# Performance work log

Measured on AMD Instinct MI355X. Metric: run time of the kernel, lower is better.

Reference implementation:

```python
import jax, jax.numpy as jnp
import numpy as np

N_NODES = 100000
N_EDGES = 1600000
IN_FEATS = 64
HIDDEN = 64
NUM_CLASSES = 40


def setup_inputs() -> dict:
    key = jax.random.key(0)
    ks = jax.random.split(key, 8)
    x = jax.random.normal(ks[0], (N_NODES, IN_FEATS), dtype=jnp.float32)
    edge_index = jax.random.randint(ks[1], (2, N_EDGES), 0, N_NODES, dtype=jnp.int64)
    s = 1.0 / np.sqrt(IN_FEATS)
    W1_l = jax.random.uniform(ks[2], (HIDDEN, IN_FEATS), jnp.float32, -s, s)
    b1 = jnp.zeros((HIDDEN,), jnp.float32)
    W1_r = jax.random.uniform(ks[3], (HIDDEN, IN_FEATS), jnp.float32, -s, s)
    s2 = 1.0 / np.sqrt(HIDDEN)
    W2_l = jax.random.uniform(ks[4], (NUM_CLASSES, HIDDEN), jnp.float32, -s2, s2)
    b2 = jnp.zeros((NUM_CLASSES,), jnp.float32)
    W2_r = jax.random.uniform(ks[5], (NUM_CLASSES, HIDDEN), jnp.float32, -s2, s2)
    return {"x": x, "edge_index": edge_index, "W1_l": W1_l, "b1": b1,
            "W1_r": W1_r, "W2_l": W2_l, "b2": b2, "W2_r": W2_r}


def _sage_conv(x, src, dst, Wl, b, Wr, num_nodes):
    # mean aggregation of source-node features onto target nodes
    msg = x[src]                                           # [E, d] gather
    agg = jax.ops.segment_sum(msg, dst, num_segments=num_nodes)   # [N, d]
    deg = jax.ops.segment_sum(jnp.ones((src.shape[0],), x.dtype), dst,
                              num_segments=num_nodes)      # [N]
    agg = agg / jnp.maximum(deg, 1.0)[:, None]
    # out = lin_l(agg) + lin_r(x)  (PyG SAGEConv: root weight, bias on lin_l)
    return agg @ Wl.T + b + x @ Wr.T


def reference(x, edge_index, W1_l, b1, W1_r, W2_l, b2, W2_r):
    n = x.shape[0]
    src, dst = edge_index[0], edge_index[1]
    h = _sage_conv(x, src, dst, W1_l, b1, W1_r, n)
    h = jax.nn.relu(h)
    # dropout p=0.5 only active in training; reference runs eval mode (identity)
    return _sage_conv(h, src, dst, W2_l, b2, W2_r, n)
```

## Files before the change

kernel.cpp:

```cpp
#include <hip/hip_runtime.h>

#define N_NODES 100000
#define N_EDGES 1600000
#define NCLS 40
#define BIN_SH 8
#define BIN_N 256
#define NBIN ((N_NODES + BIN_N - 1) / BIN_N)
#define BINCAP 4800
#define BKBLK 256
#define BKTHR 1024
#define CHUNK (N_EDGES / BKBLK)
#define SENTINEL N_NODES
#define NN1 (N_NODES + 1)

typedef __attribute__((ext_vector_type(8))) short s8v;
typedef __attribute__((ext_vector_type(4))) float f4v;

__device__ __forceinline__ unsigned short f2bf(float f) {
    union { float f; unsigned int u; } v; v.f = f;
    unsigned int u = v.u + 0x7FFFu + ((v.u >> 16) & 1u);
    return (unsigned short)(u >> 16);
}
__device__ __forceinline__ float blo(unsigned int u) {
    union { unsigned int u; float f; } v; v.u = u << 16; return v.f;
}
__device__ __forceinline__ float bhi(unsigned int u) {
    union { unsigned int u; float f; } v; v.u = u & 0xFFFF0000u; return v.f;
}

#if __has_builtin(__builtin_amdgcn_cvt_pk_fp8_f32) && __has_builtin(__builtin_amdgcn_cvt_f32_fp8)
#define FP8_HW 1
#else
#define FP8_HW 0
#endif

__device__ __forceinline__ unsigned char enc_e4m3_sw(float f) {
    union { float f; unsigned int u; } v; v.f = f;
    unsigned int s = (v.u >> 24) & 0x80u;
    float af = fabsf(f);
    if (af >= 448.0f) return (unsigned char)(s | 0x7E);
    if (af < 0.015625f) {
        int q = (int)rintf(af * 512.0f);
        return (unsigned char)(s | (q & 7));
    }
    unsigned int n = v.u & 0x7FFFFFFFu;
    n = n + 0x7FFFFu + ((n >> 20) & 1u);
    int e = (int)(n >> 23) - 120;
    unsigned int m = (n >> 20) & 7u;
    if (e <= 0) { int q = (int)rintf(af * 512.0f); return (unsigned char)(s | (q & 7)); }
    if (e > 15) return (unsigned char)(s | 0x7E);
    return (unsigned char)(s | (e << 3) | m);
}
__device__ __forceinline__ float dec_e4m3_sw(unsigned int byte) {
    unsigned int sgn = byte >> 7, e = (byte >> 3) & 15u, m = byte & 7u;
    float mag;
    if (e) { union { unsigned int u; float f; } v; v.u = ((e + 120u) << 23) | (m << 20); mag = v.f; }
    else mag = (float)m * 0.001953125f;
    return sgn ? -mag : mag;
}

__device__ __forceinline__ unsigned int pack4_fp8(float a, float b, float c, float d) {
#if FP8_HW
    unsigned int w = __builtin_amdgcn_cvt_pk_fp8_f32(a, b, 0u, false);
    w = __builtin_amdgcn_cvt_pk_fp8_f32(c, d, w, true);
    return w;
#else
    return (unsigned int)enc_e4m3_sw(a) | ((unsigned int)enc_e4m3_sw(b) << 8) |
           ((unsigned int)enc_e4m3_sw(c) << 16) | ((unsigned int)enc_e4m3_sw(d) << 24);
#endif
}
__device__ __forceinline__ void unpack4_fp8(unsigned int w, float& a, float& b, float& c, float& d) {
#if FP8_HW
    a = __builtin_amdgcn_cvt_f32_fp8(w, 0);
    b = __builtin_amdgcn_cvt_f32_fp8(w, 1);
    c = __builtin_amdgcn_cvt_f32_fp8(w, 2);
    d = __builtin_amdgcn_cvt_f32_fp8(w, 3);
#else
    a = dec_e4m3_sw(w & 255u); b = dec_e4m3_sw((w >> 8) & 255u);
    c = dec_e4m3_sw((w >> 16) & 255u); d = dec_e4m3_sw(w >> 24);
#endif
}

__global__ __launch_bounds__(BKTHR) void k_bucket(
        const int* __restrict__ srcv, const int* __restrict__ dstv,
        int* __restrict__ bcur, int* __restrict__ bedges) {
    __shared__ int cnt4[4][NBIN];
    __shared__ int base[NBIN], lcur[NBIN];
    for (int i = threadIdx.x; i < 4 * NBIN; i += BKTHR) cnt4[i / NBIN][i % NBIN] = 0;
    __syncthreads();
    const int grp = threadIdx.x >> 8;
    const int beg = blockIdx.x * CHUNK;
    const int end = beg + CHUNK;
    for (int e = beg + threadIdx.x; e < end; e += BKTHR) {
        int d = dstv[e]; d = min(max(d, 0), N_NODES - 1);
        atomicAdd(&cnt4[grp][d >> BIN_SH], 1);
    }
    __syncthreads();
    for (int i = threadIdx.x; i < NBIN; i += BKTHR) {
        int c = cnt4[0][i] + cnt4[1][i] + cnt4[2][i] + cnt4[3][i];
        base[i] = atomicAdd(&bcur[i], c);
        lcur[i] = 0;
    }
    __syncthreads();
    for (int e = beg + threadIdx.x; e < end; e += BKTHR) {
        int d = dstv[e]; d = min(max(d, 0), N_NODES - 1);
        int s = srcv[e]; s = min(max(s, 0), N_NODES - 1);
        int b = d >> BIN_SH;
        int slot = atomicAdd(&lcur[b], 1) + base[b];
        if (slot < BINCAP) bedges[b * BINCAP + slot] = ((d & (BIN_N - 1)) << 17) | s;
    }
}

__global__ __launch_bounds__(256) void k_csrfill(
        const int* __restrict__ bcur, const int* __restrict__ bedges,
        int* __restrict__ gcnt, uint2* __restrict__ offdeg,
        int* __restrict__ srcs) {
    __shared__ int dcnt[BIN_N];
    __shared__ int s[BIN_N];
    __shared__ int base_s;
    const int b = blockIdx.x;
    dcnt[threadIdx.x] = 0;
    __syncthreads();
    const int cnt = min(bcur[b], BINCAP);
    for (int e = threadIdx.x; e < cnt; e += 256)
        atomicAdd(&dcnt[bedges[b * BINCAP + e] >> 17], 1);
    __syncthreads();
    int v = dcnt[threadIdx.x];
    int pv = (v + 3) & ~3;
    s[threadIdx.x] = pv;
    __syncthreads();
    int acc = pv;
    for (int off = 1; off < 256; off <<= 1) {
        int t = (threadIdx.x >= off) ? s[threadIdx.x - off] : 0;
        __syncthreads();
        acc += t;
        s[threadIdx.x] = acc;
        __syncthreads();
    }
    if (threadIdx.x == 255) base_s = atomicAdd(gcnt, acc);
    __syncthreads();
    const int gbeg = (acc - pv) + base_s;
    const int node = (b << BIN_SH) + threadIdx.x;
    if (node < N_NODES) offdeg[node] = make_uint2((unsigned)gbeg, (unsigned)v);
    s[threadIdx.x] = gbeg;
    dcnt[threadIdx.x] = 0;
    __syncthreads();
    for (int e = threadIdx.x; e < cnt; e += 256) {
        int val = bedges[b * BINCAP + e];
        int dl = val >> 17;
        int sv = val & 0x1FFFF;
        int slot = atomicAdd(&dcnt[dl], 1);
        srcs[s[dl] + slot] = sv;
    }
    for (int p = v; p < pv; ++p) srcs[gbeg + p] = SENTINEL;
}

__global__ void k_xb(const float* __restrict__ x, unsigned int* __restrict__ xbs,
                     unsigned int* __restrict__ h2f8) {
    int i = blockIdx.x * blockDim.x + threadIdx.x;
    int stride = gridDim.x * blockDim.x;
    const int total = N_NODES * 8;
    for (int tt = i; tt < total; tt += stride) {
        int node = tt >> 3, sub = tt & 7;
        int slice = sub >> 1, half = sub & 1;
        float4 v0 = ((const float4*)x)[tt * 2];
        float4 v1 = ((const float4*)x)[tt * 2 + 1];
        uint4 o;
        o.x = (unsigned)f2bf(v0.x) | ((unsigned)f2bf(v0.y) << 16);
        o.y = (unsigned)f2bf(v0.z) | ((unsigned)f2bf(v0.w) << 16);
        o.z = (unsigned)f2bf(v1.x) | ((unsigned)f2bf(v1.y) << 16);
        o.w = (unsigned)f2bf(v1.z) | ((unsigned)f2bf(v1.w) << 16);
        ((uint4*)xbs)[((size_t)slice * NN1 + node) * 2 + half] = o;
    }
    uint4 z; z.x = 0u; z.y = 0u; z.z = 0u; z.w = 0u;
    if (i < 8) {
        int slice = i >> 1, half = i & 1;
        ((uint4*)xbs)[((size_t)slice * NN1 + N_NODES) * 2 + half] = z;
    }
    if (i >= 16 && i < 24) h2f8[(size_t)N_NODES * 8 + (i - 16)] = 0u;
    if (i >= 24 && i < 26) h2f8[8 * (size_t)NN1 + (size_t)N_NODES * 2 + (i - 24)] = 0u;
}

__global__ __launch_bounds__(256) void k_agg(
        const uint2* __restrict__ offdeg, const int* __restrict__ srcs,
        const unsigned short* __restrict__ xbs, unsigned short* __restrict__ aggs) {
    const int lane = threadIdx.x & 63;
    const int w = threadIdx.x >> 6;
    const int g = lane >> 4;
    const int c = (lane >> 2) & 3;
    const int t = lane & 3;
    const int slice = (blockIdx.x & 7) >> 1;
    const int cid = ((blockIdx.x >> 3) << 1) | (blockIdx.x & 1);
    const size_t sb = (size_t)slice * NN1;
    for (int nb = (cid * 4 + w) * 4; nb < N_NODES; nb += 8192) {
        const int node = nb + g;
        uint2 od = offdeg[node];
        const int beg = (int)od.x;
        const int m = ((int)od.y + 3) >> 2;
        float ax = 0.0f, ay = 0.0f, az = 0.0f, aw = 0.0f;
        int j = c;
        if (j < m) {
            int4 sv = *(const int4*)&srcs[beg + 4 * j];
            while (true) {
                const int4 cur = sv;
                const int jn = j + 4;
                if (jn < m) sv = *(const int4*)&srcs[beg + 4 * jn];
                uint2 u0 = *(const uint2*)&xbs[(sb + cur.x) * 16 + t * 4];
                uint2 u1 = *(const uint2*)&xbs[(sb + cur.y) * 16 + t * 4];
                uint2 u2 = *(const uint2*)&xbs[(sb + cur.z) * 16 + t * 4];
                uint2 u3 = *(const uint2*)&xbs[(sb + cur.w) * 16 + t * 4];
                ax += (blo(u0.x) + blo(u1.x)) + (blo(u2.x) + blo(u3.x));
                ay += (bhi(u0.x) + bhi(u1.x)) + (bhi(u2.x) + bhi(u3.x));
                az += (blo(u0.y) + blo(u1.y)) + (blo(u2.y) + blo(u3.y));
                aw += (bhi(u0.y) + bhi(u1.y)) + (bhi(u2.y) + bhi(u3.y));
                if (jn >= m) break;
                j = jn;
            }
        }
        ax += __shfl_xor(ax, 4, 64); ay += __shfl_xor(ay, 4, 64);
        az += __shfl_xor(az, 4, 64); aw += __shfl_xor(aw, 4, 64);
        ax += __shfl_xor(ax, 8, 64); ay += __shfl_xor(ay, 8, 64);
        az += __shfl_xor(az, 8, 64); aw += __shfl_xor(aw, 8, 64);
        if (c == 0) {
            float rd = 1.0f / fmaxf((float)od.y, 1.0f);
            uint2 r;
            r.x = (unsigned)f2bf(ax * rd) | ((unsigned)f2bf(ay * rd) << 16);
            r.y = (unsigned)f2bf(az * rd) | ((unsigned)f2bf(aw * rd) << 16);
            *(uint2*)&aggs[(sb + node) * 16 + t * 4] = r;
        }
    }
}

__global__ __launch_bounds__(256) void k_dense(
        const unsigned short* __restrict__ aggs, const unsigned short* __restrict__ xbs,
        const float* __restrict__ W1l, const float* __restrict__ b1,
        const float* __restrict__ W1r,
        const float* __restrict__ W2l, const float* __restrict__ b2,
        const float* __restrict__ W2r,
        unsigned int* __restrict__ h2f8, float* __restrict__ op) {
    __shared__ __align__(16) unsigned short wl1[64][72], wr1[64][72];
    __shared__ __align__(16) unsigned short wl2[48][72], wr2[48][72];
    __shared__ __align__(16) unsigned short hsm[4][16][72];
    for (int idx = threadIdx.x; idx < 64 * 64; idx += 256) {
        int f = idx >> 6, k = idx & 63;
        wl1[f][k] = f2bf(W1l[idx]);
        wr1[f][k] = f2bf(W1r[idx]);
    }
    for (int idx = threadIdx.x; idx < 48 * 64; idx += 256) {
        int c = idx >> 6, k = idx & 63;
        wl2[c][k] = (c < NCLS) ? f2bf(W2l[c * 64 + k]) : (unsigned short)0;
        wr2[c][k] = (c < NCLS) ? f2bf(W2r[c * 64 + k]) : (unsigned short)0;
    }
    __syncthreads();
    const int w   = threadIdx.x >> 6;
    const int l15 = threadIdx.x & 15;
    const int g   = (threadIdx.x >> 4) & 3;
    const size_t sLo = (size_t)(g >> 1) * NN1;
    const size_t sHi = (size_t)(2 + (g >> 1)) * NN1;
    const int off = (g & 1) * 8;
    float b1v[4][4], b2v[3][4];
    #pragma unroll
    for (int ft = 0; ft < 4; ++ft)
        #pragma unroll
        for (int r = 0; r < 4; ++r)
            b1v[ft][r] = b1[16 * ft + 4 * g + r];
    #pragma unroll
    for (int ct = 0; ct < 3; ++ct)
        #pragma unroll
        for (int r = 0; r < 4; ++r) {
            int c = 16 * ct + 4 * g + r;
            b2v[ct][r] = (c < NCLS) ? b2[c] : 0.0f;
        }
    unsigned short* hs = &hsm[w][0][0];
    const int gw = blockIdx.x * 4 + w;
    const int nw = gridDim.x * 4;
    for (int tile = gw; tile < N_NODES / 16; tile += nw) {
        const size_t node = (size_t)tile * 16 + l15;
        s8v aB0 = *(const s8v*)&aggs[(sLo + node) * 16 + off];
        s8v aB1 = *(const s8v*)&aggs[(sHi + node) * 16 + off];
        s8v xB0 = *(const s8v*)&xbs[(sLo + node) * 16 + off];
        s8v xB1 = *(const s8v*)&xbs[(sHi + node) * 16 + off];
        #pragma unroll
        for (int ft = 0; ft < 4; ++ft) {
            f4v c;
            c[0] = b1v[ft][0]; c[1] = b1v[ft][1]; c[2] = b1v[ft][2]; c[3] = b1v[ft][3];
            const size_t rb = (size_t)(16 * ft + l15) * 144 + 16 * g;
            s8v A0 = *(const s8v*)((const char*)wl1 + rb);
            s8v A1 = *(const s8v*)((const char*)wl1 + rb + 64);
            s8v R0 = *(const s8v*)((const char*)wr1 + rb);
            s8v R1 = *(const s8v*)((const char*)wr1 + rb + 64);
            c = __builtin_amdgcn_mfma_f32_16x16x32_bf16(A0, aB0, c, 0, 0, 0);
            c = __builtin_amdgcn_mfma_f32_16x16x32_bf16(A1, aB1, c, 0, 0, 0);
            c = __builtin_amdgcn_mfma_f32_16x16x32_bf16(R0, xB0, c, 0, 0, 0);
            c = __builtin_amdgcn_mfma_f32_16x16x32_bf16(R1, xB1, c, 0, 0, 0);
            uint2 u;
            u.x = (unsigned)f2bf(fmaxf(c[0], 0.0f)) | ((unsigned)f2bf(fmaxf(c[1], 0.0f)) << 16);
            u.y = (unsigned)f2bf(fmaxf(c[2], 0.0f)) | ((unsigned)f2bf(fmaxf(c[3], 0.0f)) << 16);
            *(uint2*)((char*)hs + l15 * 144 + 32 * ft + 8 * g) = u;
        }
        s8v hB0 = *(const s8v*)((const char*)hs + l15 * 144 + 16 * g);
        s8v hB1 = *(const s8v*)((const char*)hs + l15 * 144 + 64 + 16 * g);
        #pragma unroll
        for (int ct = 0; ct < 3; ++ct) {
            f4v p; p[0] = 0.0f; p[1] = 0.0f; p[2] = 0.0f; p[3] = 0.0f;
            f4v qv;
            qv[0] = b2v[ct][0]; qv[1] = b2v[ct][1]; qv[2] = b2v[ct][2]; qv[3] = b2v[ct][3];
            const size_t rb = (size_t)(16 * ct + l15) * 144 + 16 * g;
            s8v L0 = *(const s8v*)((const char*)wl2 + rb);
            s8v L1 = *(const s8v*)((const char*)wl2 + rb + 64);
            s8v Q0 = *(const s8v*)((const char*)wr2 + rb);
            s8v Q1 = *(const s8v*)((const char*)wr2 + rb + 64);
            p  = __builtin_amdgcn_mfma_f32_16x16x32_bf16(L0, hB0, p, 0, 0, 0);
            p  = __builtin_amdgcn_mfma_f32_16x16x32_bf16(L1, hB1, p, 0, 0, 0);
            qv = __builtin_amdgcn_mfma_f32_16x16x32_bf16(Q0, hB0, qv, 0, 0, 0);
            qv = __builtin_amdgcn_mfma_f32_16x16x32_bf16(Q1, hB1, qv, 0, 0, 0);
            int c0 = 16 * ct + 4 * g;
            if (c0 < NCLS) {
                int word = c0 >> 2;
                if (word < 8) h2f8[node * 8 + word] = pack4_fp8(p[0], p[1], p[2], p[3]);
                else h2f8[8 * (size_t)NN1 + node * 2 + (word - 8)] = pack4_fp8(p[0], p[1], p[2], p[3]);
                float4 o; o.x = qv[0]; o.y = qv[1]; o.z = qv[2]; o.w = qv[3];
                *(float4*)&op[node * NCLS + c0] = o;
            }
        }
    }
}

__global__ __launch_bounds__(256) void k_out(
        const uint2* __restrict__ offdeg, const int* __restrict__ srcs,
        const unsigned int* __restrict__ h2f8, float* __restrict__ out) {
    const int w = threadIdx.x >> 6;
    const int q = (threadIdx.x >> 4) & 3;
    const int t = threadIdx.x & 15;
    const int mul = (t < 8) ? 8 : 2;
    const unsigned add = (t < 8) ? (unsigned)t : (unsigned)(8u * NN1 + (t - 8));
    for (int node = blockIdx.x * 4 + w; node < N_NODES; node += gridDim.x * 4) {
        uint2 od = offdeg[node];
        const int beg = (int)od.x;
        const int m = ((int)od.y + 3) >> 2;
        float ax = 0.0f, ay = 0.0f, az = 0.0f, aw = 0.0f;
        if (t < 10) {
            int j = q;
            if (j < m) {
                int4 sv = *(const int4*)&srcs[beg + 4 * j];
                while (true) {
                    const int4 cur = sv;
                    const int jn = j + 4;
                    if (jn < m) sv = *(const int4*)&srcs[beg + 4 * jn];
                    unsigned u0 = h2f8[(size_t)cur.x * mul + add];
                    unsigned u1 = h2f8[(size_t)cur.y * mul + add];
                    unsigned u2 = h2f8[(size_t)cur.z * mul + add];
                    unsigned u3 = h2f8[(size_t)cur.w * mul + add];
                    float a0, b0, c0, d0, a1, b1, c1, d1;
                    float a2, b2, c2, d2, a3, b3, c3, d3;
                    unpack4_fp8(u0, a0, b0, c0, d0);
                    unpack4_fp8(u1, a1, b1, c1, d1);
                    unpack4_fp8(u2, a2, b2, c2, d2);
                    unpack4_fp8(u3, a3, b3, c3, d3);
                    ax += (a0 + a1) + (a2 + a3); ay += (b0 + b1) + (b2 + b3);
                    az += (c0 + c1) + (c2 + c3); aw += (d0 + d1) + (d2 + d3);
                    if (jn >= m) break;
                    j = jn;
                }
            }
        }
        ax += __shfl_xor(ax, 16, 64); ay += __shfl_xor(ay, 16, 64);
        az += __shfl_xor(az, 16, 64); aw += __shfl_xor(aw, 16, 64);
        ax += __shfl_xor(ax, 32, 64); ay += __shfl_xor(ay, 32, 64);
        az += __shfl_xor(az, 32, 64); aw += __shfl_xor(aw, 32, 64);
        if (q == 0 && t < 10) {
            float rd = 1.0f / fmaxf((float)od.y, 1.0f);
            float4 o = *(float4*)&out[(size_t)node * NCLS + t * 4];
            o.x = fmaf(ax, rd, o.x); o.y = fmaf(ay, rd, o.y);
            o.z = fmaf(az, rd, o.z); o.w = fmaf(aw, rd, o.w);
            *(float4*)&out[(size_t)node * NCLS + t * 4] = o;
        }
    }
}

extern "C" void kernel_launch(void* const* d_in, const int* in_sizes, int n_in,
                              void* d_out, int out_size, void* d_ws, size_t ws_size,
                              hipStream_t stream) {
    const float* x   = (const float*)d_in[0];
    const int*   ei  = (const int*)d_in[1];
    const float* W1l = (const float*)d_in[2];
    const float* b1  = (const float*)d_in[3];
    const float* W1r = (const float*)d_in[4];
    const float* W2l = (const float*)d_in[5];
    const float* b2  = (const float*)d_in[6];
    const float* W2r = (const float*)d_in[7];
    float* out = (float*)d_out;

    const int* srcv = ei;
    const int* dstv = ei + N_EDGES;

    int* bcur   = (int*)d_ws;
    int* gcnt   = bcur + 508;
    uint2* offdeg = (uint2*)(bcur + 512);
    int* bedges = (int*)(offdeg + N_NODES);
    int* srcs   = bedges + (size_t)NBIN * BINCAP;
    unsigned short* aggs = (unsigned short*)(srcs + (size_t)N_EDGES + 3 * N_NODES + 16);
    unsigned short* xbs  = aggs + (size_t)64 * NN1;
    unsigned int*   h2f8 = (unsigned int*)(xbs + (size_t)64 * NN1);

    hipMemsetAsync(bcur, 0, 512 * sizeof(int), stream);
    k_bucket<<<BKBLK, BKTHR, 0, stream>>>(srcv, dstv, bcur, bedges);
    k_xb<<<2048, 256, 0, stream>>>(x, (unsigned int*)xbs, h2f8);
    k_csrfill<<<NBIN, 256, 0, stream>>>(bcur, bedges, gcnt, offdeg, srcs);
    k_agg<<<2048, 256, 0, stream>>>(offdeg, srcs, xbs, aggs);
    k_dense<<<768, 256, 0, stream>>>(aggs, xbs, W1l, b1, W1r, W2l, b2, W2r, h2f8, out);
    k_out<<<2048, 256, 0, stream>>>(offdeg, srcs, h2f8, out);
}
```

Before: 148.2 us.

## Widen gather loads to 16 bytes in aggregation and output kernels

The first-layer aggregation now has each lane load 8 bf16 features (uint4) instead of 4, so one wave covers 8 nodes per iteration instead of 4. The second-layer fp8 buffer is laid out with a 16-word row per node, padded from 10 words, so k_out can fetch 16 fp8 values per lane with a single uint4 load and handle 4 nodes per wave. This cuts the number of gather instructions and removes the split-array addressing, at the cost of padding bytes in h2f8 and more accumulator registers, which can lower occupancy. In k_out, one of the four lanes per node slice now sits idle.

```diff
diff --git a/kernel.cpp b/kernel.cpp
--- a/kernel.cpp
+++ b/kernel.cpp
@@ -79,6 +79,20 @@
     a = dec_e4m3_sw(w & 255u); b = dec_e4m3_sw((w >> 8) & 255u);
     c = dec_e4m3_sw((w >> 16) & 255u); d = dec_e4m3_sw(w >> 24);
 #endif
+}
+
+__device__ __forceinline__ void acc_bf8(uint4 u, float* a) {
+    a[0] += blo(u.x); a[1] += bhi(u.x);
+    a[2] += blo(u.y); a[3] += bhi(u.y);
+    a[4] += blo(u.z); a[5] += bhi(u.z);
+    a[6] += blo(u.w); a[7] += bhi(u.w);
+}
+__device__ __forceinline__ void acc_fp16x(uint4 u, float* a) {
+    float f0, f1, f2, f3;
+    unpack4_fp8(u.x, f0, f1, f2, f3); a[0] += f0; a[1] += f1; a[2] += f2; a[3] += f3;
+    unpack4_fp8(u.y, f0, f1, f2, f3); a[4] += f0; a[5] += f1; a[6] += f2; a[7] += f3;
+    unpack4_fp8(u.z, f0, f1, f2, f3); a[8] += f0; a[9] += f1; a[10] += f2; a[11] += f3;
+    unpack4_fp8(u.w, f0, f1, f2, f3); a[12] += f0; a[13] += f1; a[14] += f2; a[15] += f3;
 }
 
 __global__ __launch_bounds__(BKTHR) void k_bucket(
@@ -177,8 +191,7 @@
         int slice = i >> 1, half = i & 1;
         ((uint4*)xbs)[((size_t)slice * NN1 + N_NODES) * 2 + half] = z;
     }
-    if (i >= 16 && i < 24) h2f8[(size_t)N_NODES * 8 + (i - 16)] = 0u;
-    if (i >= 24 && i < 26) h2f8[8 * (size_t)NN1 + (size_t)N_NODES * 2 + (i - 24)] = 0u;
+    if (i >= 16 && i < 28) h2f8[(size_t)N_NODES * 16 + (i - 16)] = 0u;
 }
 
 __global__ __launch_bounds__(256) void k_agg(
@@ -186,18 +199,18 @@
         const unsigned short* __restrict__ xbs, unsigned short* __restrict__ aggs) {
     const int lane = threadIdx.x & 63;
     const int w = threadIdx.x >> 6;
-    const int g = lane >> 4;
-    const int c = (lane >> 2) & 3;
-    const int t = lane & 3;
+    const int g = lane >> 3;
+    const int c = (lane >> 1) & 3;
+    const int t = lane & 1;
     const int slice = (blockIdx.x & 7) >> 1;
     const int cid = ((blockIdx.x >> 3) << 1) | (blockIdx.x & 1);
     const size_t sb = (size_t)slice * NN1;
-    for (int nb = (cid * 4 + w) * 4; nb < N_NODES; nb += 8192) {
+    for (int nb = (cid * 4 + w) * 8; nb < N_NODES; nb += 16384) {
         const int node = nb + g;
         uint2 od = offdeg[node];
         const int beg = (int)od.x;
         const int m = ((int)od.y + 3) >> 2;
-        float ax = 0.0f, ay = 0.0f, az = 0.0f, aw = 0.0f;
+        float a[8] = {0.f, 0.f, 0.f, 0.f, 0.f, 0.f, 0.f, 0.f};
         int j = c;
         if (j < m) {
             int4 sv = *(const int4*)&srcs[beg + 4 * j];
@@ -205,28 +218,28 @@
                 const int4 cur = sv;
                 const int jn = j + 4;
                 if (jn < m) sv = *(const int4*)&srcs[beg + 4 * jn];
-                uint2 u0 = *(const uint2*)&xbs[(sb + cur.x) * 16 + t * 4];
-                uint2 u1 = *(const uint2*)&xbs[(sb + cur.y) * 16 + t * 4];
-                uint2 u2 = *(const uint2*)&xbs[(sb + cur.z) * 16 + t * 4];
-                uint2 u3 = *(const uint2*)&xbs[(sb + cur.w) * 16 + t * 4];
-                ax += (blo(u0.x) + blo(u1.x)) + (blo(u2.x) + blo(u3.x));
-                ay += (bhi(u0.x) + bhi(u1.x)) + (bhi(u2.x) + bhi(u3.x));
-                az += (blo(u0.y) + blo(u1.y)) + (blo(u2.y) + blo(u3.y));
-                aw += (bhi(u0.y) + bhi(u1.y)) + (bhi(u2.y) + bhi(u3.y));
+                uint4 u0 = *(const uint4*)&xbs[(sb + cur.x) * 16 + t * 8];
+                uint4 u1 = *(const uint4*)&xbs[(sb + cur.y) * 16 + t * 8];
+                uint4 u2 = *(const uint4*)&xbs[(sb + cur.z) * 16 + t * 8];
+                uint4 u3 = *(const uint4*)&xbs[(sb + cur.w) * 16 + t * 8];
+                acc_bf8(u0, a); acc_bf8(u1, a); acc_bf8(u2, a); acc_bf8(u3, a);
                 if (jn >= m) break;
                 j = jn;
             }
         }
-        ax += __shfl_xor(ax, 4, 64); ay += __shfl_xor(ay, 4, 64);
-        az += __shfl_xor(az, 4, 64); aw += __shfl_xor(aw, 4, 64);
-        ax += __shfl_xor(ax, 8, 64); ay += __shfl_xor(ay, 8, 64);
-        az += __shfl_xor(az, 8, 64); aw += __shfl_xor(aw, 8, 64);
+        #pragma unroll
+        for (int k = 0; k < 8; ++k) {
+            a[k] += __shfl_xor(a[k], 2, 64);
+            a[k] += __shfl_xor(a[k], 4, 64);
+        }
         if (c == 0) {
             float rd = 1.0f / fmaxf((float)od.y, 1.0f);
-            uint2 r;
-            r.x = (unsigned)f2bf(ax * rd) | ((unsigned)f2bf(ay * rd) << 16);
-            r.y = (unsigned)f2bf(az * rd) | ((unsigned)f2bf(aw * rd) << 16);
-            *(uint2*)&aggs[(sb + node) * 16 + t * 4] = r;
+            uint4 r;
+            r.x = (unsigned)f2bf(a[0] * rd) | ((unsigned)f2bf(a[1] * rd) << 16);
+            r.y = (unsigned)f2bf(a[2] * rd) | ((unsigned)f2bf(a[3] * rd) << 16);
+            r.z = (unsigned)f2bf(a[4] * rd) | ((unsigned)f2bf(a[5] * rd) << 16);
+            r.w = (unsigned)f2bf(a[6] * rd) | ((unsigned)f2bf(a[7] * rd) << 16);
+            *(uint4*)&aggs[(sb + node) * 16 + t * 8] = r;
         }
     }
 }
@@ -315,10 +328,8 @@
             qv = __builtin_amdgcn_mfma_f32_16x16x32_bf16(Q0, hB0, qv, 0, 0, 0);
             qv = __builtin_amdgcn_mfma_f32_16x16x32_bf16(Q1, hB1, qv, 0, 0, 0);
             int c0 = 16 * ct + 4 * g;
+            h2f8[node * 16 + (4 * ct + g)] = pack4_fp8(p[0], p[1], p[2], p[3]);
             if (c0 < NCLS) {
-                int word = c0 >> 2;
-                if (word < 8) h2f8[node * 8 + word] = pack4_fp8(p[0], p[1], p[2], p[3]);
-                else h2f8[8 * (size_t)NN1 + node * 2 + (word - 8)] = pack4_fp8(p[0], p[1], p[2], p[3]);
                 float4 o; o.x = qv[0]; o.y = qv[1]; o.z = qv[2]; o.w = qv[3];
                 *(float4*)&op[node * NCLS + c0] = o;
             }
@@ -329,17 +340,20 @@
 __global__ __launch_bounds__(256) void k_out(
         const uint2* __restrict__ offdeg, const int* __restrict__ srcs,
         const unsigned int* __restrict__ h2f8, float* __restrict__ out) {
+    const int lane = threadIdx.x & 63;
     const int w = threadIdx.x >> 6;
-    const int q = (threadIdx.x >> 4) & 3;
-    const int t = threadIdx.x & 15;
-    const int mul = (t < 8) ? 8 : 2;
-    const unsigned add = (t < 8) ? (unsigned)t : (unsigned)(8u * NN1 + (t - 8));
-    for (int node = blockIdx.x * 4 + w; node < N_NODES; node += gridDim.x * 4) {
+    const int g = lane >> 4;
+    const int q = (lane >> 2) & 3;
+    const int t = lane & 3;
+    const int wid = blockIdx.x * 4 + w;
+    for (int nb = wid * 4; nb < N_NODES; nb += 32768) {
+        const int node = nb + g;
         uint2 od = offdeg[node];
         const int beg = (int)od.x;
         const int m = ((int)od.y + 3) >> 2;
-        float ax = 0.0f, ay = 0.0f, az = 0.0f, aw = 0.0f;
-        if (t < 10) {
+        float a[16] = {0.f, 0.f, 0.f, 0.f, 0.f, 0.f, 0.f, 0.f,
+                       0.f, 0.f, 0.f, 0.f, 0.f, 0.f, 0.f, 0.f};
+        if (t < 3) {
             int j = q;
             if (j < m) {
                 int4 sv = *(const int4*)&srcs[beg + 4 * j];
@@ -347,33 +361,37 @@
                     const int4 cur = sv;
                     const int jn = j + 4;
                     if (jn < m) sv = *(const int4*)&srcs[beg + 4 * jn];
-                    unsigned u0 = h2f8[(size_t)cur.x * mul + add];
-                    unsigned u1 = h2f8[(size_t)cur.y * mul + add];
-                    unsigned u2 = h2f8[(size_t)cur.z * mul + add];
-                    unsigned u3 = h2f8[(size_t)cur.w * mul + add];
-                    float a0, b0, c0, d0, a1, b1, c1, d1;
-                    float a2, b2, c2, d2, a3, b3, c3, d3;
-                    unpack4_fp8(u0, a0, b0, c0, d0);
-                    unpack4_fp8(u1, a1, b1, c1, d1);
-                    unpack4_fp8(u2, a2, b2, c2, d2);
-                    unpack4_fp8(u3, a3, b3, c3, d3);
-                    ax += (a0 + a1) + (a2 + a3); ay += (b0 + b1) + (b2 + b3);
-                    az += (c0 + c1) + (c2 + c3); aw += (d0 + d1) + (d2 + d3);
+                    uint4 u0 = *(const uint4*)&h2f8[(size_t)cur.x * 16 + t * 4];
+                    uint4 u1 = *(const uint4*)&h2f8[(size_t)cur.y * 16 + t * 4];
+                    uint4 u2 = *(const uint4*)&h2f8[(size_t)cur.z * 16 + t * 4];
+                    uint4 u3 = *(const uint4*)&h2f8[(size_t)cur.w * 16 + t * 4];
+                    acc_fp16x(u0, a); acc_fp16x(u1, a);
+                    acc_fp16x(u2, a); acc_fp16x(u3, a);
                     if (jn >= m) break;
                     j = jn;
                 }
             }
         }
-        ax += __shfl_xor(ax, 16, 64); ay += __shfl_xor(ay, 16, 64);
-        az += __shfl_xor(az, 16, 64); aw += __shfl_xor(aw, 16, 64);
-        ax += __shfl_xor(ax, 32, 64); ay += __shfl_xor(ay, 32, 64);
-        az += __shfl_xor(az, 32, 64); aw += __shfl_xor(aw, 32, 64);
-        if (q == 0 && t < 10) {
+        #pragma unroll
+        for (int k = 0; k < 16; ++k) {
+            a[k] += __shfl_xor(a[k], 4, 64);
+            a[k] += __shfl_xor(a[k], 8, 64);
+        }
+        if (q == 0 && t < 3) {
             float rd = 1.0f / fmaxf((float)od.y, 1.0f);
-            float4 o = *(float4*)&out[(size_t)node * NCLS + t * 4];
-            o.x = fmaf(ax, rd, o.x); o.y = fmaf(ay, rd, o.y);
-            o.z = fmaf(az, rd, o.z); o.w = fmaf(aw, rd, o.w);
-            *(float4*)&out[(size_t)node * NCLS + t * 4] = o;
+            const int base = t * 16;
+            const int nwords = (t == 2) ? 2 : 4;
+            #pragma unroll
+            for (int i = 0; i < 4; ++i) {
+                if (i < nwords) {
+                    float4 o = *(float4*)&out[(size_t)node * NCLS + base + 4 * i];
+                    o.x = fmaf(a[4 * i + 0], rd, o.x);
+                    o.y = fmaf(a[4 * i + 1], rd, o.y);
+                    o.z = fmaf(a[4 * i + 2], rd, o.z);
+                    o.w = fmaf(a[4 * i + 3], rd, o.w);
+                    *(float4*)&out[(size_t)node * NCLS + base + 4 * i] = o;
+                }
+            }
         }
     }
 }
```

New measurement: 139.7 us. 5.8% less time.
